# Performance work log

Measured on AMD Instinct MI355X. Metric: run time of the kernel, lower is better.

The kernel has to match this reference:

```python
import jax, jax.numpy as jnp
import numpy as np

B, T, I, H, O = 256, 128, 64, 2048, 24


def setup_inputs() -> dict:
    key = jax.random.key(0)
    ks = jax.random.split(key, 10)
    sI = 1.0 / np.sqrt(I)
    sH = 1.0 / np.sqrt(H)
    return {
        "trains": jax.random.normal(ks[0], (B, T, I), jnp.float32),
        "dec": jax.random.normal(ks[1], (B, O - 1), jnp.float32),
        # packed gate projections, order [i, f, o, c] along last dim
        "Wx": jax.random.normal(ks[2], (I, 4 * H), jnp.float32) * sI,
        "bx": jax.random.normal(ks[3], (4 * H,), jnp.float32) * sI,
        "Wh": jax.random.normal(ks[4], (H, 4 * H), jnp.float32) * sH,
        "bh": jax.random.normal(ks[5], (4 * H,), jnp.float32) * sH,
        "Win": jax.random.normal(ks[6], (1, I), jnp.float32),
        "b_in": jax.random.normal(ks[7], (I,), jnp.float32),
        "Wout": jax.random.normal(ks[8], (H, 1), jnp.float32) * sH,
        "bout": jax.random.normal(ks[9], (1,), jnp.float32) * sH,
    }


def reference(trains, dec, Wx, bx, Wh, bh, Win, b_in, Wout, bout):
    def cell(h, c, x):
        # fused gate GEMMs: x@Wx and h@Wh each produce all 4 gates at once
        g = x @ Wx + bx + h @ Wh + bh  # [B, 4H]
        i, f, o, cc = jnp.split(g, 4, axis=-1)
        c = jax.nn.sigmoid(f) * c + jax.nn.sigmoid(i) * jnp.tanh(cc)
        h = jax.nn.sigmoid(o) * jnp.tanh(c)
        return h, c

    b = trains.shape[0]
    hdim = Wh.shape[0]
    h0 = jnp.zeros((b, hdim), trains.dtype)
    c0 = jnp.zeros((b, hdim), trains.dtype)

    def enc_step(carry, x):
        h, c = cell(*carry, x)
        return (h, c), None

    (h, c), _ = jax.lax.scan(enc_step, (h0, c0), jnp.swapaxes(trains, 0, 1))
    y1 = h @ Wout + bout  # [B, 1]

    def dec_step(carry, x_scalar):
        x = x_scalar[:, None] @ Win + b_in  # [B, I]
        h, c = cell(*carry, x)
        return (h, c), h @ Wout + bout  # emit [B, 1]

    (h, c), ys = jax.lax.scan(dec_step, (h, c), dec.T)  # ys: [O-1, B, 1]
    return jnp.concatenate([y1, jnp.swapaxes(ys[..., 0], 0, 1)], axis=1)  # [B, O]
```

## Files before the change

kernel.cpp:

```cpp
#include <hip/hip_runtime.h>


#define NB 256
#define NH 2048
#define NI 64
#define NK 2112
#define NPK 8192
#define NSTEPS 151
#define NO 24

typedef __bf16 bf16x8 __attribute__((ext_vector_type(8)));
typedef short short8 __attribute__((ext_vector_type(8)));
typedef float f32x4 __attribute__((ext_vector_type(4)));
typedef float f32x16 __attribute__((ext_vector_type(16)));
typedef unsigned short u16;

__device__ __forceinline__ u16 f2bf(float f) {
  union { float f; unsigned u; } v; v.f = f;
  unsigned r = v.u + 0x7FFFu + ((v.u >> 16) & 1u);
  return (u16)(r >> 16);
}

__device__ __forceinline__ void gload16(const void* g, void* l) {
  __builtin_amdgcn_global_load_lds(
      (const __attribute__((address_space(1))) unsigned int*)g,
      (__attribute__((address_space(3))) unsigned int*)l, 16, 0, 0);
}

__device__ __forceinline__ float sigmoidf_(float x) { return 1.f / (1.f + __expf(-x)); }
__device__ __forceinline__ float tanhf_(float x) {
  x = fminf(15.f, fmaxf(-15.f, x));
  float e = __expf(2.f * x);
  return (e - 1.f) / (e + 1.f);
}

__global__ __launch_bounds__(256) void wl_pack_w(const float* __restrict__ Wx,
                                                 const float* __restrict__ Wh,
                                                 u16* __restrict__ Wp) {
  __shared__ float s[64][65];
  const int j0 = blockIdx.x * 64, k0 = blockIdx.y * 64;
  const int tid = threadIdx.x;
  const int jl = tid & 63, kg = tid >> 6;
#pragma unroll
  for (int it = 0; it < 16; ++it) {
    int kl = it * 4 + kg;
    int k = k0 + kl, j = j0 + jl;
    float v = (k < NH) ? Wh[(size_t)k * NPK + j] : Wx[(size_t)(k - NH) * NPK + j];
    s[kl][jl] = v;
  }
  __syncthreads();
  int j = j0 + jl;
  int p = (j & (NH - 1)) * 4 + (j >> 11);
  short8 v0, v1;
#pragma unroll
  for (int e = 0; e < 8; ++e) {
    v0[e] = (short)f2bf(s[kg * 16 + e][jl]);
    v1[e] = (short)f2bf(s[kg * 16 + 8 + e][jl]);
  }
  short8* dst = (short8*)(Wp + (size_t)p * NK + k0 + kg * 16);
  dst[0] = v0;
  dst[1] = v1;
}

__global__ __launch_bounds__(256) void wl_bsum(const float* __restrict__ bx,
                                               const float* __restrict__ bh,
                                               float* __restrict__ bsum) {
  int p = blockIdx.x * 256 + threadIdx.x;
  int j = (p & 3) * NH + (p >> 2);
  bsum[p] = bx[j] + bh[j];
}

__global__ __launch_bounds__(256) void wl_xall(const float* __restrict__ trains,
                                               const float* __restrict__ dec,
                                               const float* __restrict__ Win,
                                               const float* __restrict__ b_in,
                                               u16* __restrict__ xf) {
  int idx = blockIdx.x * 256 + threadIdx.x;
  int i = idx & 63;
  int b = (idx >> 6) & 255;
  int t = idx >> 14;
  float v;
  if (t < 128) v = trains[((size_t)b * 128 + t) * 64 + i];
  else         v = dec[b * 23 + (t - 128)] * Win[i] + b_in[i];
  size_t di = ((((size_t)t * 8 + (b >> 5)) * 4 + (i >> 4)) * 64 +
               ((i >> 3) & 1) * 32 + (b & 31)) * 8 + (i & 7);
  xf[di] = f2bf(v);
}

__global__ __launch_bounds__(256, 1) void wl_step(const u16* __restrict__ Wpg,
                                                  const float* __restrict__ bsum,
                                                  const u16* __restrict__ xf,
                                                  u16* __restrict__ hf,
                                                  float* __restrict__ c_t,
                                                  float* __restrict__ ypart,
                                                  const float* __restrict__ Wout,
                                                  int t) {
  __shared__ char arena[81920];

  const int bid = blockIdx.x;
  const int cs = (bid & 7) * 16 + ((bid >> 3) & 15);
  const int rh = bid >> 7;
  const int p0 = cs * 64, u0 = cs * 16, b0 = rh * 128;

  const int tid = threadIdx.x;
  const int wv = tid >> 6, lane = tid & 63;
  const int l31 = lane & 31, lh = lane >> 5;
  const int srow = lane >> 3, sc = lane & 7;
  const int g8 = sc ^ srow;

  const u16* __restrict__ hin = hf + (size_t)(t & 1) * (NB * NH);
  u16* __restrict__ hout = hf + (size_t)((t + 1) & 1) * (NB * NH);

  const int rbg = rh * 4 + wv;
  const u16* const ha = hin + ((size_t)(rbg * 128) * 64 + lane) * 8;
  const u16* const xa = xf + ((((size_t)t * 8 + rbg) * 4) * 64 + lane) * 8;
  const u16* const bsrc0 = Wpg + (size_t)p0 * NK;

  f32x16 acc0 = {}, acc1 = {};
  bf16x8 A[4][4];

  auto stageB = [&](int kt, int buf) {
    char* const base = arena + buf * 8192;
    const u16* bsrc = bsrc0 + (size_t)kt * 64;
#pragma unroll
    for (int i = 0; i < 2; ++i) {
      int qb = wv * 2 + i;
      int col = qb * 8 + srow;
      gload16(bsrc + (size_t)col * NK + g8 * 8, base + qb * 1024);
    }
  };
  auto loadA = [&](int kt, bf16x8* dst) {
    if (kt < 32) {
#pragma unroll
      for (int s = 0; s < 4; ++s)
        dst[s] = *(const bf16x8*)(ha + (size_t)(kt * 4 + s) * 512);
    } else {
#pragma unroll
      for (int s = 0; s < 4; ++s)
        dst[s] = *(const bf16x8*)(xa + (size_t)s * 512);
    }
  };
  auto compute = [&](int buf, bf16x8* a) {
    const char* Bb = arena + buf * 8192;
#pragma unroll
    for (int s = 0; s < 4; ++s) {
      const int c8 = s * 2 + lh;
      const int col0 = l31, col1 = 32 + l31;
      bf16x8 b0 = *(const bf16x8*)(Bb + col0 * 128 + ((c8 ^ (col0 & 7)) << 4));
      bf16x8 b1 = *(const bf16x8*)(Bb + col1 * 128 + ((c8 ^ (col1 & 7)) << 4));
      acc0 = __builtin_amdgcn_mfma_f32_32x32x16_bf16(a[s], b0, acc0, 0, 0, 0);
      acc1 = __builtin_amdgcn_mfma_f32_32x32x16_bf16(a[s], b1, acc1, 0, 0, 0);
    }
  };

  stageB(0, 0);
  stageB(1, 1); loadA(0, A[0]);
  stageB(2, 2); loadA(1, A[1]);
  stageB(3, 3); loadA(2, A[2]);
#pragma unroll
  for (int kt = 0; kt < 33; ++kt) {
    if (kt + 4 <= 32) stageB(kt + 4, (kt + 4) % 6);
    if (kt + 3 <= 32) loadA(kt + 3, A[(kt + 3) & 3]);
    if (kt <= 28)      asm volatile("s_waitcnt vmcnt(18)" ::: "memory");
    else if (kt == 29) asm volatile("s_waitcnt vmcnt(16)" ::: "memory");
    else if (kt == 30) asm volatile("s_waitcnt vmcnt(10)" ::: "memory");
    else if (kt == 31) asm volatile("s_waitcnt vmcnt(4)" ::: "memory");
    else               asm volatile("s_waitcnt vmcnt(0)" ::: "memory");
    asm volatile("s_barrier" ::: "memory");
    compute(kt % 6, A[kt & 3]);
  }

  __syncthreads();
  {
    char* const gt = arena + 49152;
#pragma unroll
    for (int cb = 0; cb < 2; ++cb) {
      const f32x16& a = cb ? acc1 : acc0;
      const int col = cb * 32 + l31;
#pragma unroll
      for (int q = 0; q < 4; ++q) {
        f32x4 v = {a[q * 4 + 0], a[q * 4 + 1], a[q * 4 + 2], a[q * 4 + 3]};
        int chunk = wv * 8 + q * 2 + lh;
        *(f32x4*)(gt + col * 512 + ((chunk ^ (col & 7)) << 4)) = v;
      }
    }
  }
  __syncthreads();

  {
    const char* const gt = arena + 49152;
    const int bl = tid & 127, ug = tid >> 7;
    const int bg = b0 + bl;
    const bool emit = (t >= 127);
    float yacc = 0.f;
    short8 hv;
#pragma unroll
    for (int j = 0; j < 8; ++j) {
      int ul = ug * 8 + j;
      float g[4];
#pragma unroll
      for (int gi = 0; gi < 4; ++gi) {
        int col = ul * 4 + gi;
        g[gi] = *(const float*)(gt + col * 512 +
                                (((bl >> 2) ^ (col & 7)) << 4) + (bl & 3) * 4);
      }
      const float4 bs = *(const float4*)(bsum + p0 + ul * 4);
      float si = sigmoidf_(g[0] + bs.x);
      float sf = sigmoidf_(g[1] + bs.y);
      float so = sigmoidf_(g[2] + bs.z);
      float tc = tanhf_(g[3] + bs.w);
      size_t ci = (size_t)(u0 + ul) * NB + bg;
      float cn = sf * c_t[ci] + si * tc;
      float h = so * tanhf_(cn);
      c_t[ci] = cn;
      hv[j] = (short)f2bf(h);
      if (emit) yacc += h * Wout[u0 + ul];
    }
    *(short8*)(hout + (((size_t)(bg >> 5) * 128 + cs) * 64 + ug * 32 + (bg & 31)) * 8) = hv;
    if (emit) ypart[((size_t)(t - 127) * 256 + cs * 2 + ug) * NB + bg] = yacc;
  }
}

__global__ __launch_bounds__(256) void wl_finy(const float* __restrict__ ypart,
                                               const float* __restrict__ bout,
                                               float* __restrict__ out) {
  int j = blockIdx.x;
  int b = threadIdx.x;
  const float* yp = ypart + (size_t)j * 256 * NB;
  float s = bout[0];
#pragma unroll 8
  for (int i = 0; i < 256; ++i) s += yp[i * NB + b];
  out[b * NO + j] = s;
}

extern "C" void kernel_launch(void* const* d_in, const int* in_sizes, int n_in,
                              void* d_out, int out_size, void* d_ws, size_t ws_size,
                              hipStream_t stream) {
  const float* trains = (const float*)d_in[0];
  const float* dec    = (const float*)d_in[1];
  const float* Wx     = (const float*)d_in[2];
  const float* bx     = (const float*)d_in[3];
  const float* Wh     = (const float*)d_in[4];
  const float* bh     = (const float*)d_in[5];
  const float* Win    = (const float*)d_in[6];
  const float* b_in   = (const float*)d_in[7];
  const float* Wout   = (const float*)d_in[8];
  const float* bout   = (const float*)d_in[9];
  float* out = (float*)d_out;
  char* ws = (char*)d_ws;

  u16*   Wp    = (u16*)(ws);
  float* bsum  = (float*)(ws + 34603008);
  u16*   xf    = (u16*)(ws + 34635776);
  u16*   hf    = (u16*)(ws + 39583744);
  float* c_t   = (float*)(ws + 41680896);
  float* ypart = (float*)(ws + 43778048);

  (void)hipMemsetAsync(ws + 39583744, 0, 4194304, stream);
  wl_pack_w<<<dim3(128, 33), 256, 0, stream>>>(Wx, Wh, Wp);
  wl_bsum<<<32, 256, 0, stream>>>(bx, bh, bsum);
  wl_xall<<<(NSTEPS * NB * NI) / 256, 256, 0, stream>>>(trains, dec, Win, b_in, xf);
  for (int t = 0; t < NSTEPS; ++t)
    wl_step<<<256, 256, 0, stream>>>(Wp, bsum, xf, hf, c_t, ypart, Wout, t);
  wl_finy<<<NO, 256, 0, stream>>>(ypart, bout, out);
}
```

Before: 2.790 ms.

## Quantize LSTM weights to int8 and use split hi/lo int8 MFMA for activations

Replaces the bf16 weight and activation path with int8. Weights get per-column scales. Activations h and x are split into hi and lo int8 parts so that i32 32x32x32 MFMAs can be used, and the results are rescaled to float in the epilogue. This halves the weight bytes streamed per step and raises MFMA throughput per byte, at the cost of twice as many MFMAs for the split operands. Weight accuracy drops to roughly 8 bits per column, which may break the tolerance check.

```diff
diff --git a/kernel.cpp b/kernel.cpp
--- a/kernel.cpp
+++ b/kernel.cpp
@@ -9,22 +9,22 @@
 #define NSTEPS 151
 #define NO 24
 
-typedef __bf16 bf16x8 __attribute__((ext_vector_type(8)));
-typedef short short8 __attribute__((ext_vector_type(8)));
+typedef int i32x4 __attribute__((ext_vector_type(4)));
+typedef int i32x16 __attribute__((ext_vector_type(16)));
 typedef float f32x4 __attribute__((ext_vector_type(4)));
-typedef float f32x16 __attribute__((ext_vector_type(16)));
 typedef unsigned short u16;
-
-__device__ __forceinline__ u16 f2bf(float f) {
-  union { float f; unsigned u; } v; v.f = f;
-  unsigned r = v.u + 0x7FFFu + ((v.u >> 16) & 1u);
-  return (u16)(r >> 16);
-}
+typedef unsigned char u8;
+typedef unsigned long long u64;
 
 __device__ __forceinline__ void gload16(const void* g, void* l) {
   __builtin_amdgcn_global_load_lds(
       (const __attribute__((address_space(1))) unsigned int*)g,
       (__attribute__((address_space(3))) unsigned int*)l, 16, 0, 0);
+}
+
+__device__ __forceinline__ int q8(float v) {
+  int q = __float2int_rn(v);
+  return q > 127 ? 127 : (q < -127 ? -127 : q);
 }
 
 __device__ __forceinline__ float sigmoidf_(float x) { return 1.f / (1.f + __expf(-x)); }
@@ -34,13 +34,35 @@
   return (e - 1.f) / (e + 1.f);
 }
 
+__global__ __launch_bounds__(256) void wl_colmax(const float* __restrict__ Wx,
+                                                 const float* __restrict__ Wh,
+                                                 float* __restrict__ sp,
+                                                 float* __restrict__ rq) {
+  __shared__ float red[4][64];
+  const int jl = threadIdx.x & 63, ks = threadIdx.x >> 6;
+  const int j = blockIdx.x * 64 + jl;
+  float m = 0.f;
+  for (int k = ks * 528; k < ks * 528 + 528; ++k) {
+    float v = (k < NH) ? Wh[(size_t)k * NPK + j] : Wx[(size_t)(k - NH) * NPK + j];
+    m = fmaxf(m, fabsf(v));
+  }
+  red[ks][jl] = m;
+  __syncthreads();
+  if (ks == 0) {
+    m = fmaxf(fmaxf(red[0][jl], red[1][jl]), fmaxf(red[2][jl], red[3][jl]));
+    int p = (j & (NH - 1)) * 4 + (j >> 11);
+    sp[p] = m * (1.f / 127.f);
+    rq[p] = (m > 0.f) ? 127.f / m : 0.f;
+  }
+}
+
 __global__ __launch_bounds__(256) void wl_pack_w(const float* __restrict__ Wx,
                                                  const float* __restrict__ Wh,
-                                                 u16* __restrict__ Wp) {
+                                                 const float* __restrict__ rq,
+                                                 u8* __restrict__ Wq) {
   __shared__ float s[64][65];
   const int j0 = blockIdx.x * 64, k0 = blockIdx.y * 64;
-  const int tid = threadIdx.x;
-  const int jl = tid & 63, kg = tid >> 6;
+  const int jl = threadIdx.x & 63, kg = threadIdx.x >> 6;
 #pragma unroll
   for (int it = 0; it < 16; ++it) {
     int kl = it * 4 + kg;
@@ -49,17 +71,14 @@
     s[kl][jl] = v;
   }
   __syncthreads();
-  int j = j0 + jl;
-  int p = (j & (NH - 1)) * 4 + (j >> 11);
-  short8 v0, v1;
-#pragma unroll
-  for (int e = 0; e < 8; ++e) {
-    v0[e] = (short)f2bf(s[kg * 16 + e][jl]);
-    v1[e] = (short)f2bf(s[kg * 16 + 8 + e][jl]);
-  }
-  short8* dst = (short8*)(Wp + (size_t)p * NK + k0 + kg * 16);
-  dst[0] = v0;
-  dst[1] = v1;
+  const int j = j0 + jl;
+  const int p = (j & (NH - 1)) * 4 + (j >> 11);
+  const int cs = p >> 6, col = p & 63;
+  const float r = rq[p];
+  union { u8 b[16]; i32x4 v; } q;
+#pragma unroll
+  for (int e = 0; e < 16; ++e) q.b[e] = (u8)(signed char)q8(s[kg * 16 + e][jl] * r);
+  *(i32x4*)(Wq + ((size_t)(cs * 33 + blockIdx.y) * 4 + kg) * 1024 + col * 16) = q.v;
 }
 
 __global__ __launch_bounds__(256) void wl_bsum(const float* __restrict__ bx,
@@ -74,28 +93,63 @@
                                                const float* __restrict__ dec,
                                                const float* __restrict__ Win,
                                                const float* __restrict__ b_in,
-                                               u16* __restrict__ xf) {
-  int idx = blockIdx.x * 256 + threadIdx.x;
-  int i = idx & 63;
-  int b = (idx >> 6) & 255;
-  int t = idx >> 14;
-  float v;
-  if (t < 128) v = trains[((size_t)b * 128 + t) * 64 + i];
-  else         v = dec[b * 23 + (t - 128)] * Win[i] + b_in[i];
-  size_t di = ((((size_t)t * 8 + (b >> 5)) * 4 + (i >> 4)) * 64 +
-               ((i >> 3) & 1) * 32 + (b & 31)) * 8 + (i & 7);
-  xf[di] = f2bf(v);
-}
-
-__global__ __launch_bounds__(256, 1) void wl_step(const u16* __restrict__ Wpg,
+                                               u8* __restrict__ xfH,
+                                               u8* __restrict__ xfL,
+                                               float* __restrict__ sx) {
+  const int t = blockIdx.x, b = threadIdx.x;
+  float x[64];
+  if (t < 128) {
+    const float4* src = (const float4*)(trains + ((size_t)b * 128 + t) * 64);
+#pragma unroll
+    for (int i = 0; i < 16; ++i) {
+      float4 v = src[i];
+      x[4 * i] = v.x; x[4 * i + 1] = v.y; x[4 * i + 2] = v.z; x[4 * i + 3] = v.w;
+    }
+  } else {
+    float d = dec[b * 23 + (t - 128)];
+#pragma unroll
+    for (int i = 0; i < 64; ++i) x[i] = d * Win[i] + b_in[i];
+  }
+  float m = 0.f;
+#pragma unroll
+  for (int i = 0; i < 64; ++i) m = fmaxf(m, fabsf(x[i]));
+  float sv, r;
+  if (m > 1e-30f) { sv = m * (1.f / 127.f); r = 127.f / m; }
+  else            { sv = 1.f; r = 0.f; }
+  sx[t * 256 + b] = sv;
+  const size_t base = (size_t)t * 16384 + (b >> 5) * 2048;
+#pragma unroll
+  for (int kc = 0; kc < 2; ++kc)
+#pragma unroll
+    for (int lhh = 0; lhh < 2; ++lhh) {
+      union { u8 b16[16]; i32x4 v; } wh, wl;
+#pragma unroll
+      for (int e = 0; e < 16; ++e) {
+        float xs = x[kc * 32 + lhh * 16 + e] * r;
+        int hi = q8(xs);
+        int lo = q8((xs - (float)hi) * 254.f);
+        wh.b16[e] = (u8)(signed char)hi;
+        wl.b16[e] = (u8)(signed char)lo;
+      }
+      size_t off = base + kc * 1024 + (lhh * 32 + (b & 31)) * 16;
+      *(i32x4*)(xfH + off) = wh.v;
+      *(i32x4*)(xfL + off) = wl.v;
+    }
+}
+
+__global__ __launch_bounds__(256, 1) void wl_step(const u8* __restrict__ Wq,
                                                   const float* __restrict__ bsum,
-                                                  const u16* __restrict__ xf,
-                                                  u16* __restrict__ hf,
+                                                  const float* __restrict__ sp,
+                                                  const u8* __restrict__ xfH,
+                                                  const u8* __restrict__ xfL,
+                                                  const float* __restrict__ sx,
+                                                  u8* __restrict__ hfH,
+                                                  u8* __restrict__ hfL,
                                                   float* __restrict__ c_t,
                                                   float* __restrict__ ypart,
                                                   const float* __restrict__ Wout,
                                                   int t) {
-  __shared__ char arena[81920];
+  __shared__ char arena[90112];
 
   const int bid = blockIdx.x;
   const int cs = (bid & 7) * 16 + ((bid >> 3) & 15);
@@ -105,95 +159,115 @@
   const int tid = threadIdx.x;
   const int wv = tid >> 6, lane = tid & 63;
   const int l31 = lane & 31, lh = lane >> 5;
-  const int srow = lane >> 3, sc = lane & 7;
-  const int g8 = sc ^ srow;
-
-  const u16* __restrict__ hin = hf + (size_t)(t & 1) * (NB * NH);
-  u16* __restrict__ hout = hf + (size_t)((t + 1) & 1) * (NB * NH);
-
-  const int rbg = rh * 4 + wv;
-  const u16* const ha = hin + ((size_t)(rbg * 128) * 64 + lane) * 8;
-  const u16* const xa = xf + ((((size_t)t * 8 + rbg) * 4) * 64 + lane) * 8;
-  const u16* const bsrc0 = Wpg + (size_t)p0 * NK;
-
-  f32x16 acc0 = {}, acc1 = {};
-  bf16x8 A[4][4];
+
+  const int par = t & 1;
+  const u8* __restrict__ hinH = hfH + (size_t)par * 524288;
+  const u8* __restrict__ hinL = hfL + (size_t)par * 524288;
+  u8* __restrict__ houtH = hfH + (size_t)(par ^ 1) * 524288;
+  u8* __restrict__ houtL = hfL + (size_t)(par ^ 1) * 524288;
+
+  const int rb = rh * 4 + wv;
+  const size_t aoff = (size_t)rb * 65536 + lane * 16;
+  const size_t xoff = (size_t)t * 16384 + rb * 2048 + lane * 16;
+  const u8* const wsrc = Wq + (size_t)cs * 135168 + wv * 1024 + lane * 16;
+
+  i32x16 aH0h = {}, aH0l = {}, aH1h = {}, aH1l = {};
+  i32x16 aX0h = {}, aX0l = {}, aX1h = {}, aX1l = {};
+  i32x4 A[4][4];
 
   auto stageB = [&](int kt, int buf) {
-    char* const base = arena + buf * 8192;
-    const u16* bsrc = bsrc0 + (size_t)kt * 64;
-#pragma unroll
-    for (int i = 0; i < 2; ++i) {
-      int qb = wv * 2 + i;
-      int col = qb * 8 + srow;
-      gload16(bsrc + (size_t)col * NK + g8 * 8, base + qb * 1024);
-    }
+    gload16(wsrc + (size_t)kt * 4096, arena + buf * 4096 + wv * 1024);
   };
-  auto loadA = [&](int kt, bf16x8* dst) {
+  auto loadA = [&](int kt, int slot) {
     if (kt < 32) {
-#pragma unroll
-      for (int s = 0; s < 4; ++s)
-        dst[s] = *(const bf16x8*)(ha + (size_t)(kt * 4 + s) * 512);
+      A[slot][0] = *(const i32x4*)(hinH + aoff + (size_t)(2 * kt) * 1024);
+      A[slot][1] = *(const i32x4*)(hinH + aoff + (size_t)(2 * kt + 1) * 1024);
+      A[slot][2] = *(const i32x4*)(hinL + aoff + (size_t)(2 * kt) * 1024);
+      A[slot][3] = *(const i32x4*)(hinL + aoff + (size_t)(2 * kt + 1) * 1024);
     } else {
-#pragma unroll
-      for (int s = 0; s < 4; ++s)
-        dst[s] = *(const bf16x8*)(xa + (size_t)s * 512);
+      A[slot][0] = *(const i32x4*)(xfH + xoff);
+      A[slot][1] = *(const i32x4*)(xfH + xoff + 1024);
+      A[slot][2] = *(const i32x4*)(xfL + xoff);
+      A[slot][3] = *(const i32x4*)(xfL + xoff + 1024);
     }
   };
-  auto compute = [&](int buf, bf16x8* a) {
-    const char* Bb = arena + buf * 8192;
-#pragma unroll
-    for (int s = 0; s < 4; ++s) {
-      const int c8 = s * 2 + lh;
-      const int col0 = l31, col1 = 32 + l31;
-      bf16x8 b0 = *(const bf16x8*)(Bb + col0 * 128 + ((c8 ^ (col0 & 7)) << 4));
-      bf16x8 b1 = *(const bf16x8*)(Bb + col1 * 128 + ((c8 ^ (col1 & 7)) << 4));
-      acc0 = __builtin_amdgcn_mfma_f32_32x32x16_bf16(a[s], b0, acc0, 0, 0, 0);
-      acc1 = __builtin_amdgcn_mfma_f32_32x32x16_bf16(a[s], b1, acc1, 0, 0, 0);
+  auto compute = [&](int kt, int buf) {
+    const char* Bb = arena + buf * 4096;
+    const int slot = kt & 3;
+#pragma unroll
+    for (int kh = 0; kh < 2; ++kh) {
+      i32x4 b0 = *(const i32x4*)(Bb + (kh * 2 + lh) * 1024 + l31 * 16);
+      i32x4 b1 = *(const i32x4*)(Bb + (kh * 2 + lh) * 1024 + (32 + l31) * 16);
+      i32x4 ah = A[slot][kh], al = A[slot][2 + kh];
+      if (kt < 32) {
+        aH0h = __builtin_amdgcn_mfma_i32_32x32x32_i8(ah, b0, aH0h, 0, 0, 0);
+        aH1h = __builtin_amdgcn_mfma_i32_32x32x32_i8(ah, b1, aH1h, 0, 0, 0);
+        aH0l = __builtin_amdgcn_mfma_i32_32x32x32_i8(al, b0, aH0l, 0, 0, 0);
+        aH1l = __builtin_amdgcn_mfma_i32_32x32x32_i8(al, b1, aH1l, 0, 0, 0);
+      } else {
+        aX0h = __builtin_amdgcn_mfma_i32_32x32x32_i8(ah, b0, aX0h, 0, 0, 0);
+        aX1h = __builtin_amdgcn_mfma_i32_32x32x32_i8(ah, b1, aX1h, 0, 0, 0);
+        aX0l = __builtin_amdgcn_mfma_i32_32x32x32_i8(al, b0, aX0l, 0, 0, 0);
+        aX1l = __builtin_amdgcn_mfma_i32_32x32x32_i8(al, b1, aX1l, 0, 0, 0);
+      }
     }
   };
 
-  stageB(0, 0);
-  stageB(1, 1); loadA(0, A[0]);
-  stageB(2, 2); loadA(1, A[1]);
-  stageB(3, 3); loadA(2, A[2]);
+  stageB(0, 0); stageB(1, 1); stageB(2, 2); stageB(3, 3);
+  loadA(0, 0); loadA(1, 1); loadA(2, 2);
 #pragma unroll
   for (int kt = 0; kt < 33; ++kt) {
     if (kt + 4 <= 32) stageB(kt + 4, (kt + 4) % 6);
-    if (kt + 3 <= 32) loadA(kt + 3, A[(kt + 3) & 3]);
-    if (kt <= 28)      asm volatile("s_waitcnt vmcnt(18)" ::: "memory");
-    else if (kt == 29) asm volatile("s_waitcnt vmcnt(16)" ::: "memory");
-    else if (kt == 30) asm volatile("s_waitcnt vmcnt(10)" ::: "memory");
+    if (kt + 3 <= 32) loadA(kt + 3, (kt + 3) & 3);
+    if (kt == 0)       asm volatile("s_waitcnt vmcnt(13)" ::: "memory");
+    else if (kt == 1)  asm volatile("s_waitcnt vmcnt(14)" ::: "memory");
+    else if (kt <= 28) asm volatile("s_waitcnt vmcnt(15)" ::: "memory");
+    else if (kt == 29) asm volatile("s_waitcnt vmcnt(14)" ::: "memory");
+    else if (kt == 30) asm volatile("s_waitcnt vmcnt(9)" ::: "memory");
     else if (kt == 31) asm volatile("s_waitcnt vmcnt(4)" ::: "memory");
     else               asm volatile("s_waitcnt vmcnt(0)" ::: "memory");
     asm volatile("s_barrier" ::: "memory");
-    compute(kt % 6, A[kt & 3]);
-  }
-
+    compute(kt, kt % 6);
+  }
+
+  {
+    char* const gH = arena + 24576;
+    char* const gX = arena + 57344;
+    const float s0 = sp[p0 + l31], s1 = sp[p0 + 32 + l31];
+#pragma unroll
+    for (int cb = 0; cb < 2; ++cb) {
+      const i32x16& ahh = cb ? aH1h : aH0h;
+      const i32x16& ahl = cb ? aH1l : aH0l;
+      const i32x16& axh = cb ? aX1h : aX0h;
+      const i32x16& axl = cb ? aX1l : aX0l;
+      const float spc = cb ? s1 : s0;
+      const float fH = spc * (1.f / 127.f);
+      const int col = cb * 32 + l31;
+#pragma unroll
+      for (int q = 0; q < 4; ++q) {
+        f32x4 vH, vX;
+#pragma unroll
+        for (int e = 0; e < 4; ++e) {
+          vH[e] = fH * ((float)ahh[4 * q + e] + (float)ahl[4 * q + e] * (1.f / 254.f));
+          vX[e] = spc * ((float)axh[4 * q + e] + (float)axl[4 * q + e] * (1.f / 254.f));
+        }
+        int chunk = wv * 8 + q * 2 + lh;
+        *(f32x4*)(gH + col * 512 + ((chunk ^ (col & 7)) << 4)) = vH;
+        *(f32x4*)(gX + col * 512 + ((chunk ^ (col & 7)) << 4)) = vX;
+      }
+    }
+  }
   __syncthreads();
+
   {
-    char* const gt = arena + 49152;
-#pragma unroll
-    for (int cb = 0; cb < 2; ++cb) {
-      const f32x16& a = cb ? acc1 : acc0;
-      const int col = cb * 32 + l31;
-#pragma unroll
-      for (int q = 0; q < 4; ++q) {
-        f32x4 v = {a[q * 4 + 0], a[q * 4 + 1], a[q * 4 + 2], a[q * 4 + 3]};
-        int chunk = wv * 8 + q * 2 + lh;
-        *(f32x4*)(gt + col * 512 + ((chunk ^ (col & 7)) << 4)) = v;
-      }
-    }
-  }
-  __syncthreads();
-
-  {
-    const char* const gt = arena + 49152;
+    const char* const gH = arena + 24576;
+    const char* const gX = arena + 57344;
     const int bl = tid & 127, ug = tid >> 7;
     const int bg = b0 + bl;
+    const float sxv = sx[t * 256 + bg];
     const bool emit = (t >= 127);
     float yacc = 0.f;
-    short8 hv;
+    union { u8 q[8]; u64 v; } hqh, hql;
 #pragma unroll
     for (int j = 0; j < 8; ++j) {
       int ul = ug * 8 + j;
@@ -201,8 +275,8 @@
 #pragma unroll
       for (int gi = 0; gi < 4; ++gi) {
         int col = ul * 4 + gi;
-        g[gi] = *(const float*)(gt + col * 512 +
-                                (((bl >> 2) ^ (col & 7)) << 4) + (bl & 3) * 4);
+        int off = col * 512 + (((bl >> 2) ^ (col & 7)) << 4) + (bl & 3) * 4;
+        g[gi] = *(const float*)(gH + off) + sxv * *(const float*)(gX + off);
       }
       const float4 bs = *(const float4*)(bsum + p0 + ul * 4);
       float si = sigmoidf_(g[0] + bs.x);
@@ -213,10 +287,17 @@
       float cn = sf * c_t[ci] + si * tc;
       float h = so * tanhf_(cn);
       c_t[ci] = cn;
-      hv[j] = (short)f2bf(h);
+      float hs = h * 127.f;
+      int hi = q8(hs);
+      int lo = q8((hs - (float)hi) * 254.f);
+      hqh.q[j] = (u8)(signed char)hi;
+      hql.q[j] = (u8)(signed char)lo;
       if (emit) yacc += h * Wout[u0 + ul];
     }
-    *(short8*)(hout + (((size_t)(bg >> 5) * 128 + cs) * 64 + ug * 32 + (bg & 31)) * 8) = hv;
+    size_t hoff = ((size_t)((bg >> 5) * 64 + (cs >> 1)) * 64 +
+                   (cs & 1) * 32 + (bg & 31)) * 16 + ug * 8;
+    *(u64*)(houtH + hoff) = hqh.v;
+    *(u64*)(houtL + hoff) = hql.v;
     if (emit) ypart[((size_t)(t - 127) * 256 + cs * 2 + ug) * NB + bg] = yacc;
   }
 }
@@ -249,18 +330,25 @@
   float* out = (float*)d_out;
   char* ws = (char*)d_ws;
 
-  u16*   Wp    = (u16*)(ws);
-  float* bsum  = (float*)(ws + 34603008);
-  u16*   xf    = (u16*)(ws + 34635776);
-  u16*   hf    = (u16*)(ws + 39583744);
-  float* c_t   = (float*)(ws + 41680896);
-  float* ypart = (float*)(ws + 43778048);
-
-  (void)hipMemsetAsync(ws + 39583744, 0, 4194304, stream);
-  wl_pack_w<<<dim3(128, 33), 256, 0, stream>>>(Wx, Wh, Wp);
+  u8*    Wq    = (u8*)(ws);
+  float* sp    = (float*)(ws + 17301504);
+  float* rq    = (float*)(ws + 17334272);
+  float* bsum  = (float*)(ws + 17367040);
+  u8*    xfH   = (u8*)(ws + 17399808);
+  u8*    xfL   = (u8*)(ws + 19873792);
+  float* sx    = (float*)(ws + 22347776);
+  u8*    hfH   = (u8*)(ws + 23550976);
+  u8*    hfL   = (u8*)(ws + 24599552);
+  float* c_t   = (float*)(ws + 25648128);
+  float* ypart = (float*)(ws + 27745280);
+
+  (void)hipMemsetAsync(ws + 23550976, 0, 4194304, stream);
+  wl_colmax<<<128, 256, 0, stream>>>(Wx, Wh, sp, rq);
+  wl_pack_w<<<dim3(128, 33), 256, 0, stream>>>(Wx, Wh, rq, Wq);
   wl_bsum<<<32, 256, 0, stream>>>(bx, bh, bsum);
-  wl_xall<<<(NSTEPS * NB * NI) / 256, 256, 0, stream>>>(trains, dec, Win, b_in, xf);
+  wl_xall<<<NSTEPS, 256, 0, stream>>>(trains, dec, Win, b_in, xfH, xfL, sx);
   for (int t = 0; t < NSTEPS; ++t)
-    wl_step<<<256, 256, 0, stream>>>(Wp, bsum, xf, hf, c_t, ypart, Wout, t);
+    wl_step<<<256, 256, 0, stream>>>(Wq, bsum, sp, xfH, xfL, sx, hfH, hfL,
+                                     c_t, ypart, Wout, t);
   wl_finy<<<NO, 256, 0, stream>>>(ypart, bout, out);
 }
```

Result: faster. 2.447 ms (-12.3%).
